# Kernel tuning notes

Measured on AMD Instinct MI355X. Metric: run time of the kernel, lower is better.

The kernel has to match this reference:

```python
import jax, jax.numpy as jnp
import numpy as np

C, N, H, OUT, NIN, NSRC, NB = 16, 8192, 181, 3, 2, 32, 8
OMEGA, SCALE = 30.0, 10.0


def _c(a):
    # view trailing dim-2 float array as complex
    return jax.lax.complex(a[..., 0], a[..., 1])


def setup_inputs() -> dict:
    key = jax.random.key(0)
    ks = jax.random.split(key, 20)
    d = {}
    d["inp"] = jax.random.normal(ks[0], (NSRC, N, NIN), jnp.float32)
    d["indices"] = jax.random.randint(ks[1], (C,), 0, NSRC)
    d["model_idx"] = jax.random.randint(ks[2], (C,), 0, C)
    d["bias_idx"] = jax.random.randint(ks[3], (C,), 0, NB)
    # first layer (real weights, in=2)
    d["W0a"] = 0.05 * jax.random.normal(ks[4], (C, NIN, H), jnp.float32)
    d["b0a"] = 0.01 * jax.random.normal(ks[5], (NB, H), jnp.float32)
    d["W0b"] = 0.05 * jax.random.normal(ks[6], (C, NIN, H), jnp.float32)
    d["b0b"] = 0.01 * jax.random.normal(ks[7], (NB, H), jnp.float32)
    # hidden complex layers stored as float[..., 2] (real, imag)
    k = 8
    for name in ["W1a", "b1a", "W1b", "b1b", "W2a", "b2a", "W2b", "b2b"]:
        if name.startswith("W"):
            d[name] = 0.01 * jax.random.normal(ks[k], (C, H, H, 2), jnp.float32)
        else:
            d[name] = 0.01 * jax.random.normal(ks[k], (NB, H, 2), jnp.float32)
        k += 1
    d["Wf"] = 0.05 * jax.random.normal(ks[16], (C, H, OUT, 2), jnp.float32)
    d["bf"] = 0.01 * jax.random.normal(ks[17], (NB, OUT, 2), jnp.float32)
    return d


def _forward(inp, indices, model_idx, bias_idx, W0a, b0a, W0b, b0b,
             W1a, b1a, W1b, b1b, W2a, b2a, W2b, b2b, Wf, bf):
    x = inp[None, indices]  # [1, C, N, in]
    # first Gabor2D layer: real adaptive linear, complex exp activation
    la = jnp.einsum('bcni,cio->bcno', x, W0a[model_idx]) + b0a[bias_idx][None, :, None, :]
    lb = jnp.einsum('bcni,cio->bcno', x, W0b[model_idx]) + b0b[bias_idx][None, :, None, :]
    # exp(1j*omega*la - |scale*la|^2 - |scale*lb|^2), la/lb real here
    x = jnp.exp(jax.lax.complex(-(SCALE * SCALE) * (la * la + lb * lb), OMEGA * la))
    # hidden Gabor2D layers: complex adaptive linear, fused Gabor chain
    for Wa, ba, Wb, bb in ((W1a, b1a, W1b, b1b), (W2a, b2a, W2b, b2b)):
        la = jnp.einsum('bcni,cio->bcno', x, _c(Wa)[model_idx]) + _c(ba)[bias_idx][None, :, None, :]
        lb = jnp.einsum('bcni,cio->bcno', x, _c(Wb)[model_idx]) + _c(bb)[bias_idx][None, :, None, :]
        # arg = 1j*omega*la - scale^2*(|la|^2 + |lb|^2)
        mag = (SCALE * SCALE) * (la.real ** 2 + la.imag ** 2 + lb.real ** 2 + lb.imag ** 2)
        x = jnp.exp(jax.lax.complex(-OMEGA * la.imag - mag, OMEGA * la.real))
    # outermost complex linear; module returns .real for complex output
    out = jnp.einsum('bcni,cio->bcno', x, _c(Wf)[model_idx]) + _c(bf)[bias_idx][None, :, None, :]
    return out.real


def reference(inp, indices, model_idx, bias_idx, W0a, b0a, W0b, b0b,
              W1a, b1a, W1b, b1b, W2a, b2a, W2b, b2b, Wf, bf):
    return _forward(inp, indices, model_idx, bias_idx, W0a, b0a, W0b, b0b,
                    W1a, b1a, W1b, b1b, W2a, b2a, W2b, b2b, Wf, bf)
```

## Files before the change

kernel.cpp:

```cpp
#include <hip/hip_runtime.h>

typedef _Float16 f16;
typedef _Float16 f16x2 __attribute__((ext_vector_type(2)));
typedef _Float16 f16x8 __attribute__((ext_vector_type(8)));
typedef float f32x4 __attribute__((ext_vector_type(4)));

namespace {

constexpr int kC = 16, kN = 8192, kH = 181, kOut = 3;
constexpr int kMB = 64;
constexpr int kKpad = 384;
constexpr int kNT = 48;
constexpr int kKS = 12;
constexpr int kRowB = 784;
constexpr float kOmega = 30.f, kS2 = 100.f;

constexpr size_t kWLayerStride = (size_t)kNT * kKS * 64 * 8;
constexpr size_t kWfOff = kWLayerStride * kC * 2;
constexpr size_t kWfStride = (size_t)kKS * 64 * 8;

__device__ __forceinline__ int xadr(int row, int colb) { return row * kRowB + colb; }

__global__ __launch_bounds__(768) void prep_hidden(
    const int* __restrict__ model_idx,
    const float* __restrict__ W1a, const float* __restrict__ W1b,
    const float* __restrict__ W2a, const float* __restrict__ W2b,
    f16* __restrict__ ws)
{
  __shared__ float s[kH][2][4][2];
  const int bid = blockIdx.x;
  const int c  = bid / (2 * kNT);
  const int L  = (bid / kNT) % 2;
  const int nt = bid % kNT;
  const int m  = model_idx[c];
  const float* Wa = (L == 0 ? W1a : W2a) + (size_t)m * kH * kH * 2;
  const float* Wb = (L == 0 ? W1b : W2b) + (size_t)m * kH * kH * 2;
  const int t = threadIdx.x;
  if (t < 2 * kH) {
    const int i = t >> 1, br = t & 1;
    const float* src = (br ? Wb : Wa) + ((size_t)i * kH + nt * 4) * 2;
#pragma unroll
    for (int e = 0; e < 8; ++e) {
      const int osub = e >> 1, reim = e & 1;
      s[i][br][osub][reim] = (nt * 4 + osub < kH) ? src[osub * 2 + reim] : 0.f;
    }
  }
  __syncthreads();
  const int ks = t >> 6, lane = t & 63;
  const int kg = lane >> 4, l15 = lane & 15;
  const int osub = l15 >> 2, comp = l15 & 3, br = comp >> 1;
  const int o = nt * 4 + osub;
  f16x8 v;
#pragma unroll
  for (int j = 0; j < 8; ++j) {
    const int k = ks * 32 + kg * 8 + j;
    float f = 0.f;
    if (k < 2 * kH && o < kH) {
      const int i = k >> 1, kodd = k & 1;
      const int reim = kodd ? (1 - (comp & 1)) : (comp & 1);
      f = s[i][br][osub][reim];
      if (kodd && !(comp & 1)) f = -f;
    }
    v[j] = (f16)f;
  }
  *(f16x8*)&ws[(((size_t)(c * 2 + L) * kNT + nt) * kKS + ks) * 512 + lane * 8] = v;
}

__global__ __launch_bounds__(768) void prep_final(
    const int* __restrict__ model_idx, const float* __restrict__ Wf,
    f16* __restrict__ ws)
{
  const int c = blockIdx.x;
  const int m = model_idx[c];
  const int t = threadIdx.x;
  const int ks = t >> 6, lane = t & 63;
  const int kg = lane >> 4, col = lane & 15;
  f16x8 v;
#pragma unroll
  for (int j = 0; j < 8; ++j) {
    const int k = ks * 32 + kg * 8 + j;
    float f = 0.f;
    if (k < 2 * kH && col < kOut) {
      const int i = k >> 1;
      const float* p = &Wf[(((size_t)m * kH + i) * kOut + col) * 2];
      f = (k & 1) ? -p[1] : p[0];
    }
    v[j] = (f16)v[j], v[j] = (f16)f;
  }
  *(f16x8*)&ws[kWfOff + ((size_t)c * kKS + ks) * 512 + lane * 8] = v;
}

__device__ __forceinline__ void hidden_gemm(
    char* __restrict__ X, const f16x8* __restrict__ wl,
    const float* __restrict__ ba, const float* __restrict__ bb,
    int w, int lane)
{
  const int kg = lane >> 4, l15 = lane & 15;
  f16x8 B[4][kKS];
#pragma unroll
  for (int pt = 0; pt < 4; ++pt)
#pragma unroll
    for (int ks = 0; ks < kKS; ++ks)
      B[pt][ks] = *(const f16x8*)(X + xadr(l15 + 16 * pt, ks * 64 + kg * 16));
  __syncthreads();

#pragma unroll 1
  for (int mi = 0; mi < 12; ++mi) {
    const int nt = w * 12 + mi;
    const int q = nt * 4 + kg;
    const f16x8* ap = wl + (size_t)nt * (kKS * 64) + lane;
    f32x4 acc[4] = {};
#pragma unroll
    for (int ks = 0; ks < kKS; ++ks) {
      const f16x8 a = ap[ks * 64];
      acc[0] = __builtin_amdgcn_mfma_f32_16x16x32_f16(a, B[0][ks], acc[0], 0, 0, 0);
      acc[1] = __builtin_amdgcn_mfma_f32_16x16x32_f16(a, B[1][ks], acc[1], 0, 0, 0);
      acc[2] = __builtin_amdgcn_mfma_f32_16x16x32_f16(a, B[2][ks], acc[2], 0, 0, 0);
      acc[3] = __builtin_amdgcn_mfma_f32_16x16x32_f16(a, B[3][ks], acc[3], 0, 0, 0);
    }
    float br_ = 0.f, bi_ = 0.f, cr_ = 0.f, ci_ = 0.f;
    if (q < kH) {
      const float2 bav = *(const float2*)&ba[q * 2];
      const float2 bbv = *(const float2*)&bb[q * 2];
      br_ = bav.x; bi_ = bav.y; cr_ = bbv.x; ci_ = bbv.y;
    }
#pragma unroll
    for (int pt = 0; pt < 4; ++pt) {
      const float v0 = acc[pt][0] + br_, v1 = acc[pt][1] + bi_;
      const float v2 = acc[pt][2] + cr_, v3 = acc[pt][3] + ci_;
      const float mag = kS2 * (v0 * v0 + v1 * v1 + v2 * v2 + v3 * v3);
      const float amp = __expf(fmaf(-kOmega, v1, -mag));
      const float ph  = kOmega * v0;
      f16x2 pv = {(f16)(amp * __cosf(ph)), (f16)(amp * __sinf(ph))};
      *(f16x2*)(X + xadr(l15 + 16 * pt, q * 4)) = pv;
    }
  }
}

__global__ __launch_bounds__(256, 2)
void wire_main(
    const float* __restrict__ inp, const int* __restrict__ indices,
    const int* __restrict__ model_idx, const int* __restrict__ bias_idx,
    const float* __restrict__ W0a, const float* __restrict__ b0a,
    const float* __restrict__ W0b, const float* __restrict__ b0b,
    const float* __restrict__ b1a, const float* __restrict__ b1b,
    const float* __restrict__ b2a, const float* __restrict__ b2b,
    const float* __restrict__ bf, const f16* __restrict__ wsW,
    float* __restrict__ out)
{
  __shared__ __align__(16) char X[kMB * kRowB];
  const int d = blockIdx.x;
  const int lg = (d & 7) * 256 + (d >> 3);
  const int c = lg >> 7;
  const int n0 = (lg & 127) * kMB;
  const int src = indices[c], m = model_idx[c], bix = bias_idx[c];
  const int tid = threadIdx.x, w = tid >> 6, lane = tid & 63;

  {
    const int r = tid >> 2, sub = tid & 3;
    const float2 xv = *(const float2*)&inp[((size_t)src * kN + n0 + r) * 2];
    const float* w0a0 = W0a + (size_t)(m * 2 + 0) * kH;
    const float* w0a1 = W0a + (size_t)(m * 2 + 1) * kH;
    const float* w0b0 = W0b + (size_t)(m * 2 + 0) * kH;
    const float* w0b1 = W0b + (size_t)(m * 2 + 1) * kH;
    const float* b0av = b0a + (size_t)bix * kH;
    const float* b0bv = b0b + (size_t)bix * kH;
    for (int t = 0; t < 48; ++t) {
      const int o = sub + 4 * t;
      float la = 0.f, lb = 0.f;
      if (o < kH) {
        la = fmaf(xv.y, w0a1[o], fmaf(xv.x, w0a0[o], b0av[o]));
        lb = fmaf(xv.y, w0b1[o], fmaf(xv.x, w0b0[o], b0bv[o]));
      }
      const float amp = __expf(-kS2 * fmaf(la, la, lb * lb));
      const float ph = kOmega * la;
      f16x2 pv = {(f16)(amp * __cosf(ph)), (f16)(amp * __sinf(ph))};
      *(f16x2*)(&X[0] + xadr(r, o * 4)) = pv;
    }
  }
  __syncthreads();
  hidden_gemm(X, (const f16x8*)(wsW + (size_t)(c * 2 + 0) * kWLayerStride),
              b1a + (size_t)bix * kH * 2, b1b + (size_t)bix * kH * 2, w, lane);
  __syncthreads();
  hidden_gemm(X, (const f16x8*)(wsW + (size_t)(c * 2 + 1) * kWLayerStride),
              b2a + (size_t)bix * kH * 2, b2b + (size_t)bix * kH * 2, w, lane);
  __syncthreads();
  {
    const int kg = lane >> 4, l15 = lane & 15;
    const f16x8* wf = (const f16x8*)(wsW + kWfOff + (size_t)c * kWfStride);
    f32x4 facc = {0.f, 0.f, 0.f, 0.f};
#pragma unroll
    for (int ks = 0; ks < kKS; ++ks) {
      f16x8 a = *(const f16x8*)(&X[0] + xadr(l15 + 16 * w, ks * 64 + kg * 16));
      f16x8 b = wf[(size_t)ks * 64 + lane];
      facc = __builtin_amdgcn_mfma_f32_16x16x32_f16(a, b, facc, 0, 0, 0);
    }
    if (l15 < kOut) {
      const float bfr = bf[(bix * kOut + l15) * 2];
#pragma unroll
      for (int j = 0; j < 4; ++j) {
        const int row = w * 16 + kg * 4 + j;
        out[((size_t)c * kN + n0 + row) * kOut + l15] = facc[j] + bfr;
      }
    }
  }
}

}

extern "C" void kernel_launch(void* const* d_in, const int* in_sizes, int n_in,
                              void* d_out, int out_size, void* d_ws, size_t ws_size,
                              hipStream_t stream) {
  const float* inp       = (const float*)d_in[0];
  const int*   indices   = (const int*)  d_in[1];
  const int*   model_idx = (const int*)  d_in[2];
  const int*   bias_idx  = (const int*)  d_in[3];
  const float* W0a = (const float*)d_in[4];
  const float* b0a = (const float*)d_in[5];
  const float* W0b = (const float*)d_in[6];
  const float* b0b = (const float*)d_in[7];
  const float* W1a = (const float*)d_in[8];
  const float* b1a = (const float*)d_in[9];
  const float* W1b = (const float*)d_in[10];
  const float* b1b = (const float*)d_in[11];
  const float* W2a = (const float*)d_in[12];
  const float* b2a = (const float*)d_in[13];
  const float* W2b = (const float*)d_in[14];
  const float* b2b = (const float*)d_in[15];
  const float* Wf  = (const float*)d_in[16];
  const float* bff = (const float*)d_in[17];
  f16*   ws  = (f16*)d_ws;
  float* out = (float*)d_out;

  prep_hidden<<<dim3(kC * 2 * kNT), dim3(768), 0, stream>>>(model_idx, W1a, W1b, W2a, W2b, ws);
  prep_final<<<dim3(kC), dim3(768), 0, stream>>>(model_idx, Wf, ws);
  wire_main<<<dim3(kC * (kN / kMB)), dim3(256), 0, stream>>>(
      inp, indices, model_idx, bias_idx, W0a, b0a, W0b, b0b,
      b1a, b1b, b2a, b2b, bff, ws, out);
}
```

Measured before the change: 219.1 us.

## Compute first layer with MFMA using prepacked f16 weights; raise priority around MFMA loops

The first real-input layer, previously scalar FMAs over global weight loads, now runs as MFMA matrix ops against a new f16 weight tile packed by an extra prep kernel. The epilogue layout matches the hidden layers, so the work is spread across waves the same way. It also adds s_setprio around the MFMA loops to favour matrix issue. In exchange there is an extra small kernel launch, and the first-layer inputs and weights are rounded to fp16, which lowers precision before the exp.

```diff
diff --git a/kernel.cpp b/kernel.cpp
--- a/kernel.cpp
+++ b/kernel.cpp
@@ -18,6 +18,8 @@
 constexpr size_t kWLayerStride = (size_t)kNT * kKS * 64 * 8;
 constexpr size_t kWfOff = kWLayerStride * kC * 2;
 constexpr size_t kWfStride = (size_t)kKS * 64 * 8;
+constexpr size_t kW0Off = kWfOff + (size_t)kC * kWfStride;
+constexpr size_t kW0Stride = (size_t)kNT * 64 * 8;
 
 __device__ __forceinline__ int xadr(int row, int colb) { return row * kRowB + colb; }
 
@@ -85,9 +87,36 @@
       const float* p = &Wf[(((size_t)m * kH + i) * kOut + col) * 2];
       f = (k & 1) ? -p[1] : p[0];
     }
-    v[j] = (f16)v[j], v[j] = (f16)f;
+    v[j] = (f16)f;
   }
   *(f16x8*)&ws[kWfOff + ((size_t)c * kKS + ks) * 512 + lane * 8] = v;
+}
+
+__global__ __launch_bounds__(256) void prep_l0(
+    const int* __restrict__ model_idx,
+    const float* __restrict__ W0a, const float* __restrict__ W0b,
+    f16* __restrict__ ws)
+{
+  const int c = blockIdx.x;
+  const int m = model_idx[c];
+#pragma unroll 1
+  for (int it = 0; it < 12; ++it) {
+    const int slot = it * 256 + threadIdx.x;
+    const int nt = slot >> 6, lane = slot & 63;
+    const int kg = lane >> 4, l15 = lane & 15;
+    const int osub = l15 >> 2, comp = l15 & 3;
+    const int o = nt * 4 + osub;
+    f16x8 v = {};
+    if (kg == 0 && o < kH && (comp & 1) == 0) {
+#pragma unroll
+      for (int k = 0; k < 2; ++k) {
+        const float f = (comp == 0) ? W0a[(m * 2 + k) * kH + o]
+                                    : W0b[(m * 2 + k) * kH + o];
+        v[k] = (f16)f;
+      }
+    }
+    *(f16x8*)&ws[kW0Off + (size_t)c * kW0Stride + (size_t)slot * 8] = v;
+  }
 }
 
 __device__ __forceinline__ void hidden_gemm(
@@ -110,6 +139,7 @@
     const int q = nt * 4 + kg;
     const f16x8* ap = wl + (size_t)nt * (kKS * 64) + lane;
     f32x4 acc[4] = {};
+    __builtin_amdgcn_s_setprio(1);
 #pragma unroll
     for (int ks = 0; ks < kKS; ++ks) {
       const f16x8 a = ap[ks * 64];
@@ -118,6 +148,7 @@
       acc[2] = __builtin_amdgcn_mfma_f32_16x16x32_f16(a, B[2][ks], acc[2], 0, 0, 0);
       acc[3] = __builtin_amdgcn_mfma_f32_16x16x32_f16(a, B[3][ks], acc[3], 0, 0, 0);
     }
+    __builtin_amdgcn_s_setprio(0);
     float br_ = 0.f, bi_ = 0.f, cr_ = 0.f, ci_ = 0.f;
     if (q < kH) {
       const float2 bav = *(const float2*)&ba[q * 2];
@@ -141,8 +172,7 @@
 void wire_main(
     const float* __restrict__ inp, const int* __restrict__ indices,
     const int* __restrict__ model_idx, const int* __restrict__ bias_idx,
-    const float* __restrict__ W0a, const float* __restrict__ b0a,
-    const float* __restrict__ W0b, const float* __restrict__ b0b,
+    const float* __restrict__ b0a, const float* __restrict__ b0b,
     const float* __restrict__ b1a, const float* __restrict__ b1b,
     const float* __restrict__ b2a, const float* __restrict__ b2b,
     const float* __restrict__ bf, const f16* __restrict__ wsW,
@@ -155,27 +185,45 @@
   const int n0 = (lg & 127) * kMB;
   const int src = indices[c], m = model_idx[c], bix = bias_idx[c];
   const int tid = threadIdx.x, w = tid >> 6, lane = tid & 63;
+  const int kg = lane >> 4, l15 = lane & 15;
 
   {
-    const int r = tid >> 2, sub = tid & 3;
-    const float2 xv = *(const float2*)&inp[((size_t)src * kN + n0 + r) * 2];
-    const float* w0a0 = W0a + (size_t)(m * 2 + 0) * kH;
-    const float* w0a1 = W0a + (size_t)(m * 2 + 1) * kH;
-    const float* w0b0 = W0b + (size_t)(m * 2 + 0) * kH;
-    const float* w0b1 = W0b + (size_t)(m * 2 + 1) * kH;
+    f16x8 Bx[4];
+#pragma unroll
+    for (int pt = 0; pt < 4; ++pt) {
+      const int row = l15 + 16 * pt;
+      const float2 xv = *(const float2*)&inp[((size_t)src * kN + n0 + row) * 2];
+      f16x8 b = {};
+      if (kg == 0) { b[0] = (f16)xv.x; b[1] = (f16)xv.y; }
+      Bx[pt] = b;
+    }
+    const f16x8* w0p = (const f16x8*)(wsW + kW0Off + (size_t)c * kW0Stride);
     const float* b0av = b0a + (size_t)bix * kH;
     const float* b0bv = b0b + (size_t)bix * kH;
-    for (int t = 0; t < 48; ++t) {
-      const int o = sub + 4 * t;
-      float la = 0.f, lb = 0.f;
-      if (o < kH) {
-        la = fmaf(xv.y, w0a1[o], fmaf(xv.x, w0a0[o], b0av[o]));
-        lb = fmaf(xv.y, w0b1[o], fmaf(xv.x, w0b0[o], b0bv[o]));
+#pragma unroll 1
+    for (int mi = 0; mi < 12; ++mi) {
+      const int nt = w * 12 + mi;
+      const int q = nt * 4 + kg;
+      const f16x8 a = w0p[nt * 64 + lane];
+      f32x4 acc[4] = {};
+      __builtin_amdgcn_s_setprio(1);
+      acc[0] = __builtin_amdgcn_mfma_f32_16x16x32_f16(a, Bx[0], acc[0], 0, 0, 0);
+      acc[1] = __builtin_amdgcn_mfma_f32_16x16x32_f16(a, Bx[1], acc[1], 0, 0, 0);
+      acc[2] = __builtin_amdgcn_mfma_f32_16x16x32_f16(a, Bx[2], acc[2], 0, 0, 0);
+      acc[3] = __builtin_amdgcn_mfma_f32_16x16x32_f16(a, Bx[3], acc[3], 0, 0, 0);
+      __builtin_amdgcn_s_setprio(0);
+      float br_ = 0.f, cr_ = 0.f;
+      if (q < kH) { br_ = b0av[q]; cr_ = b0bv[q]; }
+#pragma unroll
+      for (int pt = 0; pt < 4; ++pt) {
+        const float v0 = acc[pt][0] + br_;
+        const float v2 = acc[pt][2] + cr_;
+        const float mag = kS2 * (v0 * v0 + v2 * v2);
+        const float amp = __expf(-mag);
+        const float ph  = kOmega * v0;
+        f16x2 pv = {(f16)(amp * __cosf(ph)), (f16)(amp * __sinf(ph))};
+        *(f16x2*)(&X[0] + xadr(l15 + 16 * pt, q * 4)) = pv;
       }
-      const float amp = __expf(-kS2 * fmaf(la, la, lb * lb));
-      const float ph = kOmega * la;
-      f16x2 pv = {(f16)(amp * __cosf(ph)), (f16)(amp * __sinf(ph))};
-      *(f16x2*)(&X[0] + xadr(r, o * 4)) = pv;
     }
   }
   __syncthreads();
@@ -186,7 +234,6 @@
               b2a + (size_t)bix * kH * 2, b2b + (size_t)bix * kH * 2, w, lane);
   __syncthreads();
   {
-    const int kg = lane >> 4, l15 = lane & 15;
     const f16x8* wf = (const f16x8*)(wsW + kWfOff + (size_t)c * kWfStride);
     f32x4 facc = {0.f, 0.f, 0.f, 0.f};
 #pragma unroll
@@ -234,7 +281,8 @@
 
   prep_hidden<<<dim3(kC * 2 * kNT), dim3(768), 0, stream>>>(model_idx, W1a, W1b, W2a, W2b, ws);
   prep_final<<<dim3(kC), dim3(768), 0, stream>>>(model_idx, Wf, ws);
+  prep_l0<<<dim3(kC), dim3(256), 0, stream>>>(model_idx, W0a, W0b, ws);
   wire_main<<<dim3(kC * (kN / kMB)), dim3(256), 0, stream>>>(
-      inp, indices, model_idx, bias_idx, W0a, b0a, W0b, b0b,
+      inp, indices, model_idx, bias_idx, b0a, b0b,
       b1a, b1b, b2a, b2b, bff, ws, out);
 }
```

Measured after the change: 219.9 us. Within noise of the previous version (+0.4%).
